# Kernel tuning notes

Measured on AMD Instinct MI355X. Metric: run time of the kernel, lower is better.

## Reference

```python
import jax, jax.numpy as jnp
import numpy as np

N_HEAD = 12


def setup_inputs() -> dict:
    key = jax.random.key(0)
    ks = jax.random.split(key, 16)
    B, N, D, P, H = 1, 512, 384, 128, N_HEAD
    s = 0.02
    return {
        'x1d': jax.random.normal(ks[0], (B, N, D), jnp.float32),
        'x2d': jax.random.normal(ks[1], (B, N, N, P), jnp.float32),
        'pose_t': jax.random.normal(ks[2], (B, N, 3), jnp.float32),
        'pose_r': jax.random.normal(ks[3], (B, N, 3, 3), jnp.float32),
        'bias': jnp.zeros((B, 1, N, N), jnp.float32),
        'w_sq': jax.random.normal(ks[4], (D, D), jnp.float32) * s,
        'w_sk': jax.random.normal(ks[5], (D, D), jnp.float32) * s,
        'w_sv': jax.random.normal(ks[6], (D, D), jnp.float32) * s,
        'w_pb': jax.random.normal(ks[7], (P, H), jnp.float32) * s,
        'w_pq': jax.random.normal(ks[8], (D, H * 3 * 4), jnp.float32) * s,
        'w_pk': jax.random.normal(ks[9], (D, H * 3 * 4), jnp.float32) * s,
        'w_pv': jax.random.normal(ks[10], (D, H * 3 * 8), jnp.float32) * s,
        'tpw': jax.random.uniform(ks[11], (H,), jnp.float32),
        'w_pairv': jax.random.normal(ks[12], (P, D), jnp.float32) * s,
        'w_out': jax.random.normal(ks[13], (2 * D + H * 8 * 4, D), jnp.float32) * s,
        'b_out': jnp.zeros((D,), jnp.float32),
    }


def reference(x1d, x2d, pose_t, pose_r, bias, w_sq, w_sk, w_sv, w_pb,
              w_pq, w_pk, w_pv, tpw, w_pairv, w_out, b_out):
    B, N, D = x1d.shape
    H = N_HEAD
    dk = D // H
    scalar_w = 1.0 / np.sqrt(3 * dk)
    point_w_c = 1.0 / np.sqrt(3 * 4 * 9 / 2)
    pair_w = 1.0 / np.sqrt(3)

    T = pose_t                                # [B,N,3]
    R = jnp.swapaxes(pose_r, -1, -2)          # [B,N,3,3] (pose[1]^T as in torch code)

    # scalar attention
    q_s = (x1d @ w_sq).reshape(B, N, H, dk)
    k_s = (x1d @ w_sk).reshape(B, N, H, dk)
    v_s = (x1d @ w_sv).reshape(B, N, H, dk)
    scalar_attn = jnp.einsum('bihc,bjhc->bhij', q_s * scalar_w, k_s)

    # point attention (global frame)
    def affine(pt):  # R @ pt + T
        return jnp.einsum('bnxy,bnhpy->bnhpx', R, pt) + T[:, :, None, None, :]

    q_p = affine((x1d @ w_pq).reshape(B, N, H, 4, 3))
    k_p = affine((x1d @ w_pk).reshape(B, N, H, 4, 3))
    v_p = affine((x1d @ w_pv).reshape(B, N, H, 8, 3))

    dist = jnp.linalg.norm(q_p[:, :, None] - k_p[:, None], axis=-1)  # [B,I,J,H,P]
    pw = point_w_c * jax.nn.softplus(tpw)                            # [H]
    point_attn = -0.5 * pw[:, None, None] * jnp.transpose(dist.sum(-1), (0, 3, 1, 2))

    # pair bias attention
    pair_attn = pair_w * jnp.transpose(x2d @ w_pb, (0, 3, 1, 2))     # [B,H,I,J]

    attn = jax.nn.softmax(scalar_attn + point_attn + pair_attn + bias, axis=-1)

    # aggregations
    out_scalar = jnp.einsum('bhij,bjhc->bihc', attn, v_s).reshape(B, N, D)

    out_pg = jnp.einsum('bhij,bjhcp->bihcp', attn, v_p)              # [B,I,H,8,3]
    # inverse affine: R^T @ (x - T)
    out_pl = jnp.einsum('bnyx,bnhpy->bnhpx', R, out_pg - T[:, :, None, None, :])
    out_pn = jnp.linalg.norm(out_pl, axis=-1).reshape(B, N, H * 8)
    out_pl = out_pl.reshape(B, N, H * 8 * 3)

    v_pair = (x2d @ w_pairv).reshape(B, N, N, H, dk)
    out_pair = jnp.einsum('bhij,bijhc->bihc', attn, v_pair).reshape(B, N, D)

    feat = jnp.concatenate([out_scalar, out_pl, out_pair, out_pn], axis=-1)
    return feat @ w_out + b_out
```

## Files before the change

### kernel.cpp

```cpp
#include <hip/hip_runtime.h>
#include <hip/hip_bf16.h>
#include <math.h>

#define N_  512
#define D_  384
#define H_  12
#define DK_ 32
#define P_  128

#define PROJ_B 320
#define PAIR_B 512

typedef short short8 __attribute__((ext_vector_type(8)));
typedef float f32x4  __attribute__((ext_vector_type(4)));

static __device__ __forceinline__ unsigned short f2bf(float f) {
    union { float f; unsigned int u; } v; v.f = f;
    unsigned int r = (v.u + 0x7FFFu + ((v.u >> 16) & 1u)) >> 16;
    return (unsigned short)r;
}
static __device__ __forceinline__ float bf2f(unsigned short u) {
    union { unsigned int u; float f; } v; v.u = ((unsigned int)u) << 16;
    return v.f;
}
static __device__ __forceinline__ short2 pk2bf(float a, float b) {
    __hip_bfloat162 h = __float22bfloat162_rn(make_float2(a, b));
    return *(short2*)&h;
}
typedef union { short8 v; short2 h2[4]; } s8u;

__global__ __launch_bounds__(384, 3) void k_front(
    const float* __restrict__ x2d, const float* __restrict__ w_pb,
    float* __restrict__ pairlog,
    const float* __restrict__ x1d, const float* __restrict__ pose_t,
    const float* __restrict__ pose_r,
    const float* __restrict__ w_sq, const float* __restrict__ w_sk,
    const float* __restrict__ w_sv, const float* __restrict__ w_pq,
    const float* __restrict__ w_pk, const float* __restrict__ w_pv,
    float* __restrict__ qs, float* __restrict__ kst,
    float* __restrict__ qp, float* __restrict__ kpt,
    unsigned short* __restrict__ vcatT)
{
    __shared__ float smem[12288];

    const int t = threadIdx.x;

    if (blockIdx.x >= PROJ_B) {
        const int pb   = blockIdx.x - PROJ_B;
        const int wid  = t >> 6;
        const int lane = t & 63;
        const int quad = lane >> 4;
        const int col  = lane & 15;
        const int gw   = pb * 6 + wid;
        const float pair_w = 0.57735027f;

        float* wl = smem + wid * 2048;

        short8 bfr[4];
        #pragma unroll
        for (int kt = 0; kt < 4; ++kt) {
            #pragma unroll
            for (int jj = 0; jj < 8; ++jj) {
                int p = kt * 32 + quad * 8 + jj;
                bfr[kt][jj] = (col < 12) ? (short)f2bf(w_pb[p * 12 + col]) : (short)0;
            }
        }

        auto LDT = [&](float4* f, int T) {
            const float* tb = x2d + ((size_t)((T >> 5) * N_ + ((T & 31) << 4))) * P_;
            #pragma unroll
            for (int k = 0; k < 8; ++k)
                f[k] = *(const float4*)(tb + k * 256 + lane * 4);
        };
        auto CMP = [&](const float4* f, int T, bool dostore) {
            #pragma unroll
            for (int k = 0; k < 8; ++k) {
                int off  = k * 1024 + lane * 16;
                int soff = off ^ (((off >> 9) & 7) << 4);
                *(float4*)((char*)wl + soff) = f[k];
            }
            f32x4 acc = {0.f, 0.f, 0.f, 0.f};
            #pragma unroll
            for (int kt = 0; kt < 4; ++kt) {
                int g0 = (col * 512 + kt * 128 + quad * 32) ^ ((col & 7) << 4);
                float4 x0 = *(const float4*)((const char*)wl + g0);
                float4 x1 = *(const float4*)((const char*)wl + (g0 ^ 16));
                s8u afr;
                afr.h2[0] = pk2bf(x0.x, x0.y);
                afr.h2[1] = pk2bf(x0.z, x0.w);
                afr.h2[2] = pk2bf(x1.x, x1.y);
                afr.h2[3] = pk2bf(x1.z, x1.w);
                acc = __builtin_amdgcn_mfma_f32_16x16x32_bf16(afr.v, bfr[kt], acc, 0, 0, 0);
            }
            if (dostore && col < 12) {
                const int i  = T >> 5;
                const int j0 = (T & 31) << 4;
                float4 st = make_float4(pair_w * acc[0], pair_w * acc[1],
                                        pair_w * acc[2], pair_w * acc[3]);
                *(float4*)(pairlog + ((size_t)(col * N_ + i)) * N_ + j0 + quad * 4) = st;
            }
        };

        const bool has6 = (gw + 15360) < 16384;
        const int  T5   = has6 ? (gw + 15360) : gw;

        float4 fA[8], fB[8], fC[8];
        LDT(fA, gw);
        LDT(fB, gw + 3072);
        LDT(fC, gw + 6144);   CMP(fA, gw,          true);
        LDT(fA, gw + 9216);   CMP(fB, gw + 3072,   true);
        LDT(fB, gw + 12288);  CMP(fC, gw + 6144,   true);
        LDT(fC, T5);          CMP(fA, gw + 9216,   true);
        CMP(fB, gw + 12288, true);
        CMP(fC, T5, has6);
        return;
    }

    float (*raw)[288] = reinterpret_cast<float(*)[288]>(smem);
    float (*Rsh)[9]   = reinterpret_cast<float(*)[9]>(smem + 2304);
    float (*Tsh)[3]   = reinterpret_cast<float(*)[3]>(smem + 2304 + 72);

    const int b   = blockIdx.x;
    const int seg = b >> 6;
    const int i0  = (b & 63) * 8;

    if (seg < 3) {
        const float* __restrict__ w = (seg == 0) ? w_sq : (seg == 1) ? w_sk : w_sv;
        float acc[8];
        #pragma unroll
        for (int r = 0; r < 8; ++r) acc[r] = 0.f;
        for (int d = 0; d < D_; d += 4) {
            float4 xr[8];
            #pragma unroll
            for (int r = 0; r < 8; ++r)
                xr[r] = *(const float4*)(x1d + (i0 + r) * D_ + d);
            #pragma unroll
            for (int e = 0; e < 4; ++e) {
                float wv = w[(d + e) * D_ + t];
                #pragma unroll
                for (int r = 0; r < 8; ++r)
                    acc[r] += ((const float*)&xr[r])[e] * wv;
            }
        }
        if (seg == 0) {
            #pragma unroll
            for (int r = 0; r < 8; ++r) qs[(i0 + r) * D_ + t] = acc[r];
        } else if (seg == 1) {
            *(float4*)(kst + t * N_ + i0)     = make_float4(acc[0], acc[1], acc[2], acc[3]);
            *(float4*)(kst + t * N_ + i0 + 4) = make_float4(acc[4], acc[5], acc[6], acc[7]);
        } else {
            int h = t >> 5, c = t & 31;
            s8u sv;
            #pragma unroll
            for (int r = 0; r < 4; ++r) sv.h2[r] = pk2bf(acc[2*r], acc[2*r+1]);
            *(short8*)(vcatT + ((size_t)h * 64 + c) * N_ + i0) = sv.v;
        }
    } else {
        if (t < 72) Rsh[t / 9][t % 9] = pose_r[(i0 + t / 9) * 9 + t % 9];
        else if (t < 96) {
            int r = (t - 72) / 3, c = (t - 72) % 3;
            Tsh[r][c] = pose_t[(i0 + r) * 3 + c];
        }

        if (t < 288) {
            const float* __restrict__ w;
            int col, ldw;
            if (seg == 3) {
                if (t < 144) { w = w_pq; col = t;       ldw = 144; }
                else         { w = w_pk; col = t - 144; ldw = 144; }
            } else         { w = w_pv; col = t;       ldw = 288; }
            float acc[8];
            #pragma unroll
            for (int r = 0; r < 8; ++r) acc[r] = 0.f;
            for (int d = 0; d < D_; d += 4) {
                float4 xr[8];
                #pragma unroll
                for (int r = 0; r < 8; ++r)
                    xr[r] = *(const float4*)(x1d + (i0 + r) * D_ + d);
                #pragma unroll
                for (int e = 0; e < 4; ++e) {
                    float wv = w[(d + e) * ldw + col];
                    #pragma unroll
                    for (int r = 0; r < 8; ++r)
                        acc[r] += ((const float*)&xr[r])[e] * wv;
                }
            }
            #pragma unroll
            for (int r = 0; r < 8; ++r) raw[r][t] = acc[r];
        }
        __syncthreads();

        if (t < 288) {
            const int x3   = t % 3;
            const int base = t - x3;
            if (seg == 3) {
                const int c = (t < 144) ? t : t - 144;
                if (t < 144) {
                    #pragma unroll
                    for (int r = 0; r < 8; ++r) {
                        float g = Rsh[r][0 + x3] * raw[r][base]
                                + Rsh[r][3 + x3] * raw[r][base + 1]
                                + Rsh[r][6 + x3] * raw[r][base + 2] + Tsh[r][x3];
                        qp[(i0 + r) * 144 + c] = g;
                    }
                } else {
                    float g[8];
                    #pragma unroll
                    for (int r = 0; r < 8; ++r)
                        g[r] = Rsh[r][0 + x3] * raw[r][base]
                             + Rsh[r][3 + x3] * raw[r][base + 1]
                             + Rsh[r][6 + x3] * raw[r][base + 2] + Tsh[r][x3];
                    *(float4*)(kpt + c * N_ + i0)     = make_float4(g[0], g[1], g[2], g[3]);
                    *(float4*)(kpt + c * N_ + i0 + 4) = make_float4(g[4], g[5], g[6], g[7]);
                }
            } else {
                int h = t / 24, pc = t % 24;
                float g[8];
                #pragma unroll
                for (int r = 0; r < 8; ++r)
                    g[r] = Rsh[r][0 + x3] * raw[r][base]
                         + Rsh[r][3 + x3] * raw[r][base + 1]
                         + Rsh[r][6 + x3] * raw[r][base + 2] + Tsh[r][x3];
                s8u sv;
                #pragma unroll
                for (int r = 0; r < 4; ++r) sv.h2[r] = pk2bf(g[2*r], g[2*r+1]);
                *(short8*)(vcatT + ((size_t)h * 64 + 32 + pc) * N_ + i0) = sv.v;
            }
        }
    }
}

__global__ __launch_bounds__(256) void k_sp_soft(
    const float* __restrict__ qs, const float* __restrict__ kst,
    const float* __restrict__ qp, const float* __restrict__ kpt,
    const float* __restrict__ bias, const float* __restrict__ tpw,
    const float* __restrict__ pairlog,
    unsigned short* __restrict__ attn_bf)
{
    const int h  = blockIdx.x / 128;
    const int i0 = (blockIdx.x % 128) * 4;
    const int t  = threadIdx.x;
    const int lane = t & 63;
    const int wid  = t >> 6;
    __shared__ float qsh[4][32];
    __shared__ float qph[4][12];
    __shared__ float wredm[4][4];
    __shared__ float wreds[4][4];
    if (t < 128) { int il = t / 32, c = t % 32; qsh[il][c] = qs[(i0+il) * D_ + h*32 + c]; }
    else if (t < 176) { int r = t - 128; int il = r / 12, c = r % 12; qph[il][c] = qp[(i0+il)*144 + h*12 + c]; }
    const float pwh = 0.13608276f * log1pf(expf(tpw[h]));
    const float scalar_w = 0.10206207f;
    __syncthreads();

    float v[4][2];
    for (int jh = 0; jh < 2; ++jh) {
        int j = t + jh * 256;
        float kv[32];
        #pragma unroll
        for (int c = 0; c < 32; ++c) kv[c] = kst[(h*32 + c) * N_ + j];
        float kp[12];
        #pragma unroll
        for (int c = 0; c < 12; ++c) kp[c] = kpt[(h*12 + c) * N_ + j];

        #pragma unroll
        for (int il = 0; il < 4; ++il) {
            float s = 0.f;
            #pragma unroll
            for (int c = 0; c < 32; ++c) s += qsh[il][c] * kv[c];
            float dsum = 0.f;
            #pragma unroll
            for (int p = 0; p < 4; ++p) {
                float dx = qph[il][p*3+0] - kp[p*3+0];
                float dy = qph[il][p*3+1] - kp[p*3+1];
                float dz = qph[il][p*3+2] - kp[p*3+2];
                dsum += sqrtf(dx*dx + dy*dy + dz*dz);
            }
            v[il][jh] = scalar_w * s - 0.5f * pwh * dsum
                      + bias[(i0+il) * N_ + j]
                      + pairlog[((size_t)(h * N_ + (i0+il))) * N_ + j];
        }
    }

    #pragma unroll
    for (int il = 0; il < 4; ++il) {
        float mt = fmaxf(v[il][0], v[il][1]);
        #pragma unroll
        for (int off = 1; off < 64; off <<= 1)
            mt = fmaxf(mt, __shfl_xor(mt, off));
        if (lane == 0) wredm[il][wid] = mt;
    }
    __syncthreads();
    float m[4];
    #pragma unroll
    for (int il = 0; il < 4; ++il)
        m[il] = fmaxf(fmaxf(wredm[il][0], wredm[il][1]),
                      fmaxf(wredm[il][2], wredm[il][3]));

    #pragma unroll
    for (int il = 0; il < 4; ++il) {
        float e0 = __expf(v[il][0] - m[il]);
        float e1 = __expf(v[il][1] - m[il]);
        v[il][0] = e0; v[il][1] = e1;
        float st = e0 + e1;
        #pragma unroll
        for (int off = 1; off < 64; off <<= 1)
            st += __shfl_xor(st, off);
        if (lane == 0) wreds[il][wid] = st;
    }
    __syncthreads();
    #pragma unroll
    for (int il = 0; il < 4; ++il) {
        float inv = 1.0f / (wreds[il][0] + wreds[il][1] + wreds[il][2] + wreds[il][3]);
        size_t base = ((size_t)(h * N_ + i0 + il)) * N_;
        attn_bf[base + t]       = f2bf(v[il][0] * inv);
        attn_bf[base + t + 256] = f2bf(v[il][1] * inv);
    }
}

__global__ __launch_bounds__(256) void k_mid(
    const unsigned short* __restrict__ attn_bf,
    const float* __restrict__ x2d,
    const unsigned short* __restrict__ vcatT,
    float* __restrict__ tmp,
    float* __restrict__ feat, float* __restrict__ outpg)
{
    __shared__ float4 at[3][N_];
    __shared__ float red[4][1536];

    const int t = threadIdx.x;

    if (blockIdx.x < 512) {
        const int i = blockIdx.x;
        for (int idx = t; idx < 12 * N_; idx += 256) {
            int h = idx >> 9, j = idx & 511;
            float a = bf2f(attn_bf[((size_t)(h * N_ + i)) * N_ + j]);
            ((float*)&at[h >> 2][j])[h & 3] = a;
        }
        __syncthreads();

        const int p2 = (t & 63) * 2;
        const int jh = t >> 6;
        float acc[12][2];
        #pragma unroll
        for (int h = 0; h < 12; ++h) { acc[h][0] = 0.f; acc[h][1] = 0.f; }
        const float* xb = x2d + (size_t)i * N_ * P_;

        #pragma unroll 4
        for (int j = jh; j < N_; j += 4) {
            float2 x = *(const float2*)(xb + j * P_ + p2);
            float4 a0 = at[0][j], a1 = at[1][j], a2 = at[2][j];
            acc[0][0]  += a0.x*x.x; acc[0][1]  += a0.x*x.y;
            acc[1][0]  += a0.y*x.x; acc[1][1]  += a0.y*x.y;
            acc[2][0]  += a0.z*x.x; acc[2][1]  += a0.z*x.y;
            acc[3][0]  += a0.w*x.x; acc[3][1]  += a0.w*x.y;
            acc[4][0]  += a1.x*x.x; acc[4][1]  += a1.x*x.y;
            acc[5][0]  += a1.y*x.x; acc[5][1]  += a1.y*x.y;
            acc[6][0]  += a1.z*x.x; acc[6][1]  += a1.z*x.y;
            acc[7][0]  += a1.w*x.x; acc[7][1]  += a1.w*x.y;
            acc[8][0]  += a2.x*x.x; acc[8][1]  += a2.x*x.y;
            acc[9][0]  += a2.y*x.x; acc[9][1]  += a2.y*x.y;
            acc[10][0] += a2.z*x.x; acc[10][1] += a2.z*x.y;
            acc[11][0] += a2.w*x.x; acc[11][1] += a2.w*x.y;
        }
        #pragma unroll
        for (int h = 0; h < 12; ++h) {
            red[jh][h * 128 + p2]     = acc[h][0];
            red[jh][h * 128 + p2 + 1] = acc[h][1];
        }
        __syncthreads();
        for (int idx = t; idx < 1536; idx += 256)
            tmp[(size_t)i * 1536 + idx] = red[0][idx] + red[1][idx] + red[2][idx] + red[3][idx];
        return;
    }

    const int bid  = blockIdx.x - 512;
    const int h    = bid >> 5;
    const int i0   = (bid & 31) << 4;
    const int wid  = t >> 6;
    const int lane = t & 63;
    const int quad = lane >> 4;
    const int col  = lane & 15;
    const int c    = wid * 16 + col;
    const bool cvalid = (c < 56);

    const unsigned short* arow = attn_bf + ((size_t)(h * N_ + i0 + col)) * N_;
    const unsigned short* brow = vcatT + ((size_t)h * 64 + c) * N_;

    f32x4 acc = {0.f, 0.f, 0.f, 0.f};
    #pragma unroll
    for (int kt = 0; kt < 16; ++kt) {
        const int k0 = kt * 32 + quad * 8;
        short8 a = *(const short8*)(arow + k0);
        short8 b;
        if (cvalid) b = *(const short8*)(brow + k0);
        else { b[0]=0;b[1]=0;b[2]=0;b[3]=0;b[4]=0;b[5]=0;b[6]=0;b[7]=0; }
        acc = __builtin_amdgcn_mfma_f32_16x16x32_bf16(a, b, acc, 0, 0, 0);
    }
    #pragma unroll
    for (int r = 0; r < 4; ++r) {
        int i = i0 + quad * 4 + r;
        if (c < 32)       feat[(size_t)i * 1152 + h * 32 + c] = acc[r];
        else if (c < 56)  outpg[((size_t)i * 12 + h) * 24 + (c - 32)] = acc[r];
    }
}

__global__ __launch_bounds__(384) void k_feat(
    const float* __restrict__ tmp, const float* __restrict__ outpg,
    const float* __restrict__ pose_t, const float* __restrict__ pose_r,
    const float* __restrict__ w_pairv, float* __restrict__ feat)
{
    const int i = blockIdx.x;
    const int t = threadIdx.x;
    __shared__ float tsh[1536];
    __shared__ float pg[288];
    __shared__ float pl[288];
    __shared__ float Rsh[9], Tsh[3];

    for (int idx = t; idx < 1536; idx += 384) tsh[idx] = tmp[(size_t)i * 1536 + idx];
    if (t < 288) pg[t] = outpg[i * 288 + t];
    if (t < 9) Rsh[t] = pose_r[i * 9 + t];
    if (t < 3) Tsh[t] = pose_t[i * 3 + t];
    __syncthreads();

    {
        int h = t >> 5;
        const float* ts = tsh + h * 128;
        float acc = 0.f;
        #pragma unroll 4
        for (int p = 0; p < 128; ++p) acc += ts[p] * w_pairv[p * D_ + t];
        feat[(size_t)i * 1152 + 672 + t] = acc;
    }
    if (t < 288) {
        int x3 = t % 3, base = t - x3;
        float g0 = pg[base + 0] - Tsh[0];
        float g1 = pg[base + 1] - Tsh[1];
        float g2 = pg[base + 2] - Tsh[2];
        float v = Rsh[x3*3+0]*g0 + Rsh[x3*3+1]*g1 + Rsh[x3*3+2]*g2;
        pl[t] = v;
        feat[(size_t)i * 1152 + 384 + t] = v;
    }
    __syncthreads();
    if (t < 96) {
        float a = pl[t*3], b = pl[t*3+1], c = pl[t*3+2];
        feat[(size_t)i * 1152 + 1056 + t] = sqrtf(a*a + b*b + c*c);
    }
}

__global__ __launch_bounds__(384) void k_out_part(
    const float* __restrict__ feat, const float* __restrict__ w_out,
    float* __restrict__ part)
{
    const int kc = blockIdx.x >> 6;
    const int i0 = (blockIdx.x & 63) * 8;
    const int t  = threadIdx.x;
    const int k0 = kc * 144;

    float acc[8];
    #pragma unroll
    for (int r = 0; r < 8; ++r) acc[r] = 0.f;

    for (int d = 0; d < 144; d += 4) {
        float4 fr[8];
        #pragma unroll
        for (int r = 0; r < 8; ++r)
            fr[r] = *(const float4*)(feat + (size_t)(i0 + r) * 1152 + k0 + d);
        #pragma unroll
        for (int e = 0; e < 4; ++e) {
            float wv = w_out[(size_t)(k0 + d + e) * D_ + t];
            #pragma unroll
            for (int r = 0; r < 8; ++r)
                acc[r] += ((const float*)&fr[r])[e] * wv;
        }
    }
    #pragma unroll
    for (int r = 0; r < 8; ++r)
        part[((size_t)kc * N_ + i0 + r) * D_ + t] = acc[r];
}

__global__ __launch_bounds__(256) void k_out_red(
    const float* __restrict__ part, const float* __restrict__ b_out,
    float* __restrict__ out)
{
    const int idx = blockIdx.x * 256 + threadIdx.x;
    float s = b_out[idx % D_];
    #pragma unroll
    for (int kc = 0; kc < 8; ++kc) s += part[(size_t)kc * (N_ * D_) + idx];
    out[idx] = s;
}

extern "C" void kernel_launch(void* const* d_in, const int* in_sizes, int n_in,
                              void* d_out, int out_size, void* d_ws, size_t ws_size,
                              hipStream_t stream)
{
    (void)in_sizes; (void)n_in; (void)out_size; (void)ws_size;
    const float* x1d     = (const float*)d_in[0];
    const float* x2d     = (const float*)d_in[1];
    const float* pose_t  = (const float*)d_in[2];
    const float* pose_r  = (const float*)d_in[3];
    const float* bias    = (const float*)d_in[4];
    const float* w_sq    = (const float*)d_in[5];
    const float* w_sk    = (const float*)d_in[6];
    const float* w_sv    = (const float*)d_in[7];
    const float* w_pb    = (const float*)d_in[8];
    const float* w_pq    = (const float*)d_in[9];
    const float* w_pk    = (const float*)d_in[10];
    const float* w_pv    = (const float*)d_in[11];
    const float* tpw     = (const float*)d_in[12];
    const float* w_pairv = (const float*)d_in[13];
    const float* w_out   = (const float*)d_in[14];
    const float* b_out   = (const float*)d_in[15];
    float* out = (float*)d_out;

    float* ws = (float*)d_ws;
    float* qs      = ws;
    float* kst     = qs      + 196608;
    float* qp      = kst     + 196608;
    float* kpt     = qp      + 73728;
    float* pairlog = kpt     + 73728;
    float* tmp     = pairlog + 3145728;
    float* outpg   = tmp     + 786432;
    float* feat    = outpg   + 147456;
    float* part    = feat    + 589824;
    unsigned short* attn_bf = (unsigned short*)(part + 1572864);
    unsigned short* vcatT   = attn_bf + (size_t)12 * N_ * N_;

    hipLaunchKernelGGL(k_front, dim3(PROJ_B + PAIR_B), dim3(384), 0, stream,
                       x2d, w_pb, pairlog,
                       x1d, pose_t, pose_r, w_sq, w_sk, w_sv, w_pq, w_pk, w_pv,
                       qs, kst, qp, kpt, vcatT);
    hipLaunchKernelGGL(k_sp_soft, dim3(12 * 128), dim3(256), 0, stream,
                       qs, kst, qp, kpt, bias, tpw, pairlog, attn_bf);
    hipLaunchKernelGGL(k_mid, dim3(512 + 384), dim3(256), 0, stream,
                       attn_bf, x2d, vcatT, tmp, feat, outpg);
    hipLaunchKernelGGL(k_feat, dim3(N_), dim3(384), 0, stream,
                       tmp, outpg, pose_t, pose_r, w_pairv, feat);
    hipLaunchKernelGGL(k_out_part, dim3(512), dim3(384), 0, stream,
                       feat, w_out, part);
    hipLaunchKernelGGL(k_out_red, dim3(768), dim3(256), 0, stream,
                       part, b_out, out);
}
```

Measured before the change: 407.6 us.

## Stream x2d tiles directly into LDS via global_load_lds with single-buffer prefetch

The pair-bias branch now loads x2d tiles straight from global memory into LDS with global_load_lds, applying the swizzle on the source address, instead of staging them through registers (three register buffers of 8 float4). A loop reads the LDS tile into registers, issues the prefetch of the next tile into the same LDS buffer, then runs the MFMA. This cuts register pressure, so the launch bounds drop the min-blocks hint. In exchange there is less load lookahead: only one tile is in flight, down from roughly two, which may expose HBM latency on this bandwidth-bound x2d read.

```diff
diff --git a/kernel.cpp b/kernel.cpp
--- a/kernel.cpp
+++ b/kernel.cpp
@@ -14,6 +14,9 @@
 typedef short short8 __attribute__((ext_vector_type(8)));
 typedef float f32x4  __attribute__((ext_vector_type(4)));
 
+typedef const __attribute__((address_space(1))) void GAS;
+typedef __attribute__((address_space(3))) void LAS;
+
 static __device__ __forceinline__ unsigned short f2bf(float f) {
     union { float f; unsigned int u; } v; v.f = f;
     unsigned int r = (v.u + 0x7FFFu + ((v.u >> 16) & 1u)) >> 16;
@@ -29,7 +32,7 @@
 }
 typedef union { short8 v; short2 h2[4]; } s8u;
 
-__global__ __launch_bounds__(384, 3) void k_front(
+__global__ __launch_bounds__(384) void k_front(
     const float* __restrict__ x2d, const float* __restrict__ w_pb,
     float* __restrict__ pairlog,
     const float* __restrict__ x1d, const float* __restrict__ pose_t,
@@ -66,53 +69,59 @@
             }
         }
 
-        auto LDT = [&](float4* f, int T) {
-            const float* tb = x2d + ((size_t)((T >> 5) * N_ + ((T & 31) << 4))) * P_;
-            #pragma unroll
-            for (int k = 0; k < 8; ++k)
-                f[k] = *(const float4*)(tb + k * 256 + lane * 4);
+        auto GLL = [&](int T) {
+            const char* tb = (const char*)(x2d
+                + ((size_t)((T >> 5) * N_ + ((T & 31) << 4))) * P_);
+            #pragma unroll
+            for (int k = 0; k < 8; ++k) {
+                int q   = k * 1024 + lane * 16;
+                int src = q ^ (((q >> 9) & 7) << 4);
+                __builtin_amdgcn_global_load_lds(
+                    (GAS*)(tb + src),
+                    (LAS*)((char*)wl + k * 1024),
+                    16, 0, 0);
+            }
         };
-        auto CMP = [&](const float4* f, int T, bool dostore) {
-            #pragma unroll
-            for (int k = 0; k < 8; ++k) {
-                int off  = k * 1024 + lane * 16;
-                int soff = off ^ (((off >> 9) & 7) << 4);
-                *(float4*)((char*)wl + soff) = f[k];
-            }
-            f32x4 acc = {0.f, 0.f, 0.f, 0.f};
+
+        const bool has6 = (gw + 15360) < 16384;
+        const int  nt   = has6 ? 6 : 5;
+
+        int T = gw;
+        GLL(T);
+        for (int s = 0; s < nt; ++s) {
+            asm volatile("s_waitcnt vmcnt(0)" ::: "memory");
+
+            float4 xf[8];
             #pragma unroll
             for (int kt = 0; kt < 4; ++kt) {
                 int g0 = (col * 512 + kt * 128 + quad * 32) ^ ((col & 7) << 4);
-                float4 x0 = *(const float4*)((const char*)wl + g0);
-                float4 x1 = *(const float4*)((const char*)wl + (g0 ^ 16));
+                xf[2*kt]   = *(const float4*)((const char*)wl + g0);
+                xf[2*kt+1] = *(const float4*)((const char*)wl + (g0 ^ 16));
+            }
+            asm volatile("s_waitcnt lgkmcnt(0)" ::: "memory");
+
+            const int Tn = T + 3072;
+            if (s + 1 < nt) GLL(Tn);
+
+            f32x4 acc = {0.f, 0.f, 0.f, 0.f};
+            #pragma unroll
+            for (int kt = 0; kt < 4; ++kt) {
                 s8u afr;
-                afr.h2[0] = pk2bf(x0.x, x0.y);
-                afr.h2[1] = pk2bf(x0.z, x0.w);
-                afr.h2[2] = pk2bf(x1.x, x1.y);
-                afr.h2[3] = pk2bf(x1.z, x1.w);
+                afr.h2[0] = pk2bf(xf[2*kt].x,   xf[2*kt].y);
+                afr.h2[1] = pk2bf(xf[2*kt].z,   xf[2*kt].w);
+                afr.h2[2] = pk2bf(xf[2*kt+1].x, xf[2*kt+1].y);
+                afr.h2[3] = pk2bf(xf[2*kt+1].z, xf[2*kt+1].w);
                 acc = __builtin_amdgcn_mfma_f32_16x16x32_bf16(afr.v, bfr[kt], acc, 0, 0, 0);
             }
-            if (dostore && col < 12) {
+            if (col < 12) {
                 const int i  = T >> 5;
                 const int j0 = (T & 31) << 4;
                 float4 st = make_float4(pair_w * acc[0], pair_w * acc[1],
                                         pair_w * acc[2], pair_w * acc[3]);
                 *(float4*)(pairlog + ((size_t)(col * N_ + i)) * N_ + j0 + quad * 4) = st;
             }
-        };
-
-        const bool has6 = (gw + 15360) < 16384;
-        const int  T5   = has6 ? (gw + 15360) : gw;
-
-        float4 fA[8], fB[8], fC[8];
-        LDT(fA, gw);
-        LDT(fB, gw + 3072);
-        LDT(fC, gw + 6144);   CMP(fA, gw,          true);
-        LDT(fA, gw + 9216);   CMP(fB, gw + 3072,   true);
-        LDT(fB, gw + 12288);  CMP(fC, gw + 6144,   true);
-        LDT(fC, T5);          CMP(fA, gw + 9216,   true);
-        CMP(fB, gw + 12288, true);
-        CMP(fC, T5, has6);
+            T = Tn;
+        }
         return;
     }
 
```

After: 351.2 us, median of 2. -13.8%, faster.
